# Optimization experiments

Measured on AMD Instinct MI355X. Metric: run time of the kernel, lower is better.

## Reference

```python
import jax, jax.numpy as jnp
import numpy as np

EPS = 1e-12

def _l2norm(x):
    # F.normalize(p=2, dim=-1) with torch's eps clamp
    n = jnp.sqrt(jnp.sum(x * x, axis=-1, keepdims=True))
    return x / jnp.maximum(n, EPS)

def setup_inputs() -> dict:
    key = jax.random.key(0)
    k1, k2, k3, k4 = jax.random.split(key, 4)
    B, Lq, Ld, H, D = 64, 32, 256, 768, 128
    Q_hidden = jax.random.normal(k1, (B, Lq, H), dtype=jnp.float32)
    D_hidden = jax.random.normal(k2, (B, Ld, H), dtype=jnp.float32)
    W = jax.random.normal(k3, (D, H), dtype=jnp.float32) * (1.0 / np.sqrt(H))
    d_mask = jax.random.randint(k4, (B, Ld), 0, 2).astype(bool)
    d_mask = d_mask.at[:, 0].set(True)  # every doc has >=1 valid token
    return {"Q_hidden": Q_hidden, "D_hidden": D_hidden, "W": W, "d_mask": d_mask}

def reference(Q_hidden, D_hidden, W, d_mask):
    # linear projection (no bias) + L2 normalize, as in query()/doc()
    Q = _l2norm(jnp.einsum('blh,dh->bld', Q_hidden, W))       # [B,Lq,D]
    Dv = _l2norm(jnp.einsum('blh,dh->bld', D_hidden, W))      # [B,Ld,D]
    Dv = Dv * d_mask[..., None].astype(Dv.dtype)              # zero padded/skiplist tokens
    # intra-batch cosine MaxSim: sim[b,c,q,n] = Q[b,q] . D[c,n]
    sim = jnp.einsum('bqd,cnd->bcqn', Q, Dv)                  # [B,B,Lq,Ld]
    sim = jnp.where(d_mask[None, :, None, :], sim, -jnp.inf)  # mask doc tokens
    return jnp.sum(jnp.max(sim, axis=-1), axis=-1)            # [B,B]
```

## Files before the change

### kernel.cpp

```cpp
#include <hip/hip_runtime.h>
#include <hip/hip_bf16.h>
#include <math.h>

typedef __attribute__((ext_vector_type(4))) float f32x4;
typedef __attribute__((ext_vector_type(8))) short bf16x8;

#define NB    64
#define LQ    32
#define LDOC  256
#define HDIM  768
#define DDIM  128
#define NTOK_Q (NB * LQ)
#define NTOK_D (NB * LDOC)
#define NTOK   (NTOK_Q + NTOK_D)

#define WS_OFF_W    0
#define WS_OFF_MASK 196608
#define WS_OFF_QN   212992
#define WS_OFF_DN   737280

__device__ inline short f2bf(float f) {
    unsigned u = __float_as_uint(f);
    u = (u + 0x7fffu + ((u >> 16) & 1u)) >> 16;
    return (short)u;
}

__global__ void prep(const float* __restrict__ W, short* __restrict__ Wbf,
                     const unsigned char* __restrict__ mraw,
                     unsigned short* __restrict__ maskT) {
    if (blockIdx.x < 96) {
        int i = blockIdx.x * 256 + threadIdx.x;
        float4 v = *(const float4*)(W + (size_t)i * 4);
        short4 o;
        o.x = f2bf(v.x); o.y = f2bf(v.y); o.z = f2bf(v.z); o.w = f2bf(v.w);
        *(short4*)(Wbf + (size_t)i * 4) = o;
        return;
    }
    __shared__ int dword_ok_s;
    if (threadIdx.x == 0) dword_ok_s = 1;
    __syncthreads();
    const unsigned* dw = (const unsigned*)mraw;
    int ok = 1;
    for (int i = threadIdx.x; i < 4096; i += 256) {
        unsigned v = dw[i];
        if (!(v == 0u || v == 1u || v == 0x3F800000u)) ok = 0;
    }
    if (!ok) atomicAnd(&dword_ok_s, 0);
    __syncthreads();
    const int isdw = dword_ok_s;
    for (int w = threadIdx.x; w < 1024; w += 256) {
        const int c = w >> 4, lcc = w & 15;
        unsigned bits = 0;
        if (isdw) {
            for (int nt = 0; nt < 16; ++nt)
                bits |= (dw[c * 256 + nt * 16 + lcc] ? 1u : 0u) << nt;
        } else {
            for (int nt = 0; nt < 16; ++nt)
                bits |= (mraw[c * 256 + nt * 16 + lcc] ? 1u : 0u) << nt;
        }
        maskT[w] = (unsigned short)bits;
    }
}

__global__ __launch_bounds__(256)
void proj_norm(const float* __restrict__ Qh, const float* __restrict__ Dh,
               const short* __restrict__ Wbf,
               short* __restrict__ Qn, short* __restrict__ Dn) {
    const int tid  = threadIdx.x;
    const int lane = tid & 63;
    const int wave = tid >> 6;
    const int g    = lane >> 4;
    const int lc   = lane & 15;
    const int wr   = wave >> 1;
    const int wc   = wave & 1;
    const int row0 = blockIdx.x * 64;

    const float* Asrc = (row0 < NTOK_Q) ? Qh + (size_t)row0 * HDIM
                                        : Dh + (size_t)(row0 - NTOK_Q) * HDIM;

    __shared__ alignas(16) float As[2][4096];
    __shared__ alignas(16) short Bs[2][8192];
    __shared__ float norms[2][2][32];

    auto STAGE = [&](int buf, int t) {
#pragma unroll
        for (int i = 0; i < 4; ++i) {
            const int sb = i * 256 + wave * 64;
            const int s  = sb + lane;
            const int row = s >> 4;
            const int cu  = (s & 15) ^ (row & 15);
            const float* ga = Asrc + (size_t)row * HDIM + t * 64 + cu * 4;
            __builtin_amdgcn_global_load_lds(
                (const __attribute__((address_space(1))) unsigned*)ga,
                (__attribute__((address_space(3))) unsigned*)((char*)&As[buf][0] + (size_t)sb * 16),
                16, 0, 0);
        }
#pragma unroll
        for (int i = 0; i < 4; ++i) {
            const int sb = i * 256 + wave * 64;
            const int s  = sb + lane;
            const int n  = s >> 3;
            const int c8 = (s & 7) ^ (n & 7);
            const short* gb = Wbf + (size_t)n * HDIM + t * 64 + c8 * 8;
            __builtin_amdgcn_global_load_lds(
                (const __attribute__((address_space(1))) unsigned*)gb,
                (__attribute__((address_space(3))) unsigned*)((char*)&Bs[buf][0] + (size_t)sb * 16),
                16, 0, 0);
        }
    };

    f32x4 acc[2][4];
#pragma unroll
    for (int m = 0; m < 2; ++m)
#pragma unroll
        for (int nt = 0; nt < 4; ++nt) acc[m][nt] = (f32x4){0.f, 0.f, 0.f, 0.f};

    STAGE(0, 0);
    __syncthreads();

    for (int t = 0; t < 12; ++t) {
        const int cur = t & 1;
        if (t < 11) STAGE(cur ^ 1, t + 1);

        const float* Ab = &As[cur][0];
        const short* Bb = &Bs[cur][0];
#pragma unroll
        for (int ks = 0; ks < 2; ++ks) {
            bf16x8 bfr[4];
#pragma unroll
            for (int nt = 0; nt < 4; ++nt) {
                const int nl = wc * 64 + nt * 16 + lc;
                const int c8 = (ks * 4 + g) ^ (nl & 7);
                bfr[nt] = *(const bf16x8*)(Bb + (size_t)nl * 64 + c8 * 8);
            }
#pragma unroll
            for (int m = 0; m < 2; ++m) {
                const int rl = wr * 32 + m * 16 + lc;
                const int u0 = (ks * 8 + g * 2) ^ lc;
                const int u1 = (ks * 8 + g * 2 + 1) ^ lc;
                const float4 a0 = *(const float4*)(Ab + (size_t)rl * 64 + u0 * 4);
                const float4 a1 = *(const float4*)(Ab + (size_t)rl * 64 + u1 * 4);
                bf16x8 af;
                af[0] = f2bf(a0.x); af[1] = f2bf(a0.y); af[2] = f2bf(a0.z); af[3] = f2bf(a0.w);
                af[4] = f2bf(a1.x); af[5] = f2bf(a1.y); af[6] = f2bf(a1.z); af[7] = f2bf(a1.w);
#pragma unroll
                for (int nt = 0; nt < 4; ++nt)
                    acc[m][nt] = __builtin_amdgcn_mfma_f32_16x16x32_bf16(af, bfr[nt], acc[m][nt], 0, 0, 0);
            }
        }
        __syncthreads();
    }

    float part[2][4];
#pragma unroll
    for (int m = 0; m < 2; ++m)
#pragma unroll
        for (int i = 0; i < 4; ++i) {
            float s = 0.f;
#pragma unroll
            for (int nt = 0; nt < 4; ++nt) s += acc[m][nt][i] * acc[m][nt][i];
            s += __shfl_xor(s, 1);
            s += __shfl_xor(s, 2);
            s += __shfl_xor(s, 4);
            s += __shfl_xor(s, 8);
            part[m][i] = s;
        }
    if (lc == 0) {
#pragma unroll
        for (int m = 0; m < 2; ++m)
#pragma unroll
            for (int i = 0; i < 4; ++i)
                norms[wr][wc][m * 16 + g * 4 + i] = part[m][i];
    }
    __syncthreads();

    short* Obase = (row0 < NTOK_Q) ? Qn + (size_t)row0 * DDIM
                                   : Dn + (size_t)(row0 - NTOK_Q) * DDIM;
#pragma unroll
    for (int m = 0; m < 2; ++m)
#pragma unroll
        for (int i = 0; i < 4; ++i) {
            const int rloc = m * 16 + g * 4 + i;
            const float tot = norms[wr][0][rloc] + norms[wr][1][rloc];
            const float inv = 1.f / fmaxf(sqrtf(tot), 1e-12f);
            short* dst = Obase + (size_t)(wr * 32 + rloc) * DDIM + wc * 64;
#pragma unroll
            for (int nt = 0; nt < 4; ++nt)
                dst[nt * 16 + lc] = f2bf(acc[m][nt][i] * inv);
        }
}

__global__ __launch_bounds__(256)
void maxsim(const short* __restrict__ Qn, const short* __restrict__ Dn,
            const unsigned short* __restrict__ maskT, float* __restrict__ out) {
    const int x  = blockIdx.x & 7;
    const int m8 = (blockIdx.x >> 3) & 7;
    const int bg = blockIdx.x >> 6;
    const int c  = x * 8 + m8;

    const int wave = threadIdx.x >> 6;
    const int lane = threadIdx.x & 63;
    const int g = lane >> 4, lc = lane & 15;

    __shared__ alignas(16) short Ds[LDOC * DDIM];

    const short* dsrc = Dn + (size_t)c * LDOC * DDIM;
#pragma unroll
    for (int i = 0; i < 16; ++i) {
        const int slot = wave * 1024 + i * 64 + lane;
        const int row = slot >> 4, c16 = slot & 15;
        const short* gaddr = dsrc + row * DDIM + ((c16 ^ (row & 15)) * 8);
        __builtin_amdgcn_global_load_lds(
            (const __attribute__((address_space(1))) unsigned int*)gaddr,
            (__attribute__((address_space(3))) unsigned int*)(Ds + (size_t)(wave * 1024 + i * 64) * 8),
            16, 0, 0);
    }

    bf16x8 qf[4][4];
    const int qrow0 = bg * 256 + wave * 64;
#pragma unroll
    for (int m = 0; m < 4; ++m) {
        const short* qb = Qn + (size_t)(qrow0 + m * 16 + lc) * DDIM;
#pragma unroll
        for (int ks = 0; ks < 4; ++ks)
            qf[m][ks] = *(const bf16x8*)(qb + ks * 32 + g * 8);
    }

    const unsigned mbits = maskT[c * 16 + lc];

    __syncthreads();

    float rmax[4][4];
#pragma unroll
    for (int m = 0; m < 4; ++m)
#pragma unroll
        for (int i = 0; i < 4; ++i) rmax[m][i] = -INFINITY;

    for (int nt = 0; nt < 16; ++nt) {
        bf16x8 bf[4];
        const int row = nt * 16 + lc;
#pragma unroll
        for (int ks = 0; ks < 4; ++ks) {
            const int c16 = (ks * 4 + g) ^ lc;
            bf[ks] = *(const bf16x8*)(Ds + row * DDIM + c16 * 8);
        }
        const bool on = (mbits >> nt) & 1;
#pragma unroll
        for (int m = 0; m < 4; ++m) {
            f32x4 acc = (f32x4){0.f, 0.f, 0.f, 0.f};
#pragma unroll
            for (int ks = 0; ks < 4; ++ks)
                acc = __builtin_amdgcn_mfma_f32_16x16x32_bf16(qf[m][ks], bf[ks], acc, 0, 0, 0);
#pragma unroll
            for (int i = 0; i < 4; ++i)
                rmax[m][i] = on ? fmaxf(rmax[m][i], acc[i]) : rmax[m][i];
        }
    }

    float s_lo = 0.f, s_hi = 0.f;
#pragma unroll
    for (int m = 0; m < 4; ++m) {
#pragma unroll
        for (int i = 0; i < 4; ++i) {
            float r = rmax[m][i];
            r = fmaxf(r, __shfl_xor(r, 1));
            r = fmaxf(r, __shfl_xor(r, 2));
            r = fmaxf(r, __shfl_xor(r, 4));
            r = fmaxf(r, __shfl_xor(r, 8));
            if (m < 2) s_lo += r; else s_hi += r;
        }
    }
    s_lo += __shfl_xor(s_lo, 16);
    s_lo += __shfl_xor(s_lo, 32);
    s_hi += __shfl_xor(s_hi, 16);
    s_hi += __shfl_xor(s_hi, 32);

    if (lane == 0) {
        const int b_lo = bg * 8 + wave * 2;
        out[(size_t)b_lo * NB + c]       = s_lo;
        out[(size_t)(b_lo + 1) * NB + c] = s_hi;
    }
}

extern "C" void kernel_launch(void* const* d_in, const int* in_sizes, int n_in,
                              void* d_out, int out_size, void* d_ws, size_t ws_size,
                              hipStream_t stream) {
    const float* Qh = (const float*)d_in[0];
    const float* Dh = (const float*)d_in[1];
    const float* W  = (const float*)d_in[2];
    const unsigned char* dm = (const unsigned char*)d_in[3];
    float* out = (float*)d_out;
    char* ws = (char*)d_ws;

    short*          Wbf   = (short*)(ws + WS_OFF_W);
    unsigned short* maskT = (unsigned short*)(ws + WS_OFF_MASK);
    short*          Qn    = (short*)(ws + WS_OFF_QN);
    short*          Dn    = (short*)(ws + WS_OFF_DN);

    prep<<<97, 256, 0, stream>>>(W, Wbf, dm, maskT);
    proj_norm<<<NTOK / 64, 256, 0, stream>>>(Qh, Dh, Wbf, Qn, Dn);
    maxsim<<<512, 256, 0, stream>>>(Qn, Dn, maskT, out);
}
```

Baseline: 50.36 us.

## Halve projection row tile and pipeline doc chunks in maxsim with 512 threads

proj_norm now processes 32 rows per block instead of 64, which doubles the grid (576 blocks) and roughly halves the A-tile LDS and accumulator registers. maxsim now uses 8 waves per block with 32 query rows each and streams the 256-token doc tile in four double-buffered 64-row chunks instead of loading the whole 64KB tile up front. The aim is more resident blocks and overlap of doc loads with MFMA work. In exchange, W-tile traffic per output row doubles in the projection, and maxsim adds per-chunk barriers.

Result: faster. 42.63 us (-15.4%).

```diff
diff --git a/kernel.cpp b/kernel.cpp
--- a/kernel.cpp
+++ b/kernel.cpp
@@ -73,18 +73,18 @@
     const int lc   = lane & 15;
     const int wr   = wave >> 1;
     const int wc   = wave & 1;
-    const int row0 = blockIdx.x * 64;
+    const int row0 = blockIdx.x * 32;
 
     const float* Asrc = (row0 < NTOK_Q) ? Qh + (size_t)row0 * HDIM
                                         : Dh + (size_t)(row0 - NTOK_Q) * HDIM;
 
-    __shared__ alignas(16) float As[2][4096];
+    __shared__ alignas(16) float As[2][2048];
     __shared__ alignas(16) short Bs[2][8192];
-    __shared__ float norms[2][2][32];
+    __shared__ float norms[2][2][16];
 
     auto STAGE = [&](int buf, int t) {
 #pragma unroll
-        for (int i = 0; i < 4; ++i) {
+        for (int i = 0; i < 2; ++i) {
             const int sb = i * 256 + wave * 64;
             const int s  = sb + lane;
             const int row = s >> 4;
@@ -109,11 +109,9 @@
         }
     };
 
-    f32x4 acc[2][4];
-#pragma unroll
-    for (int m = 0; m < 2; ++m)
-#pragma unroll
-        for (int nt = 0; nt < 4; ++nt) acc[m][nt] = (f32x4){0.f, 0.f, 0.f, 0.f};
+    f32x4 acc[4];
+#pragma unroll
+    for (int nt = 0; nt < 4; ++nt) acc[nt] = (f32x4){0.f, 0.f, 0.f, 0.f};
 
     STAGE(0, 0);
     __syncthreads();
@@ -133,64 +131,54 @@
                 const int c8 = (ks * 4 + g) ^ (nl & 7);
                 bfr[nt] = *(const bf16x8*)(Bb + (size_t)nl * 64 + c8 * 8);
             }
-#pragma unroll
-            for (int m = 0; m < 2; ++m) {
-                const int rl = wr * 32 + m * 16 + lc;
-                const int u0 = (ks * 8 + g * 2) ^ lc;
-                const int u1 = (ks * 8 + g * 2 + 1) ^ lc;
-                const float4 a0 = *(const float4*)(Ab + (size_t)rl * 64 + u0 * 4);
-                const float4 a1 = *(const float4*)(Ab + (size_t)rl * 64 + u1 * 4);
-                bf16x8 af;
-                af[0] = f2bf(a0.x); af[1] = f2bf(a0.y); af[2] = f2bf(a0.z); af[3] = f2bf(a0.w);
-                af[4] = f2bf(a1.x); af[5] = f2bf(a1.y); af[6] = f2bf(a1.z); af[7] = f2bf(a1.w);
-#pragma unroll
-                for (int nt = 0; nt < 4; ++nt)
-                    acc[m][nt] = __builtin_amdgcn_mfma_f32_16x16x32_bf16(af, bfr[nt], acc[m][nt], 0, 0, 0);
-            }
+            const int rl = wr * 16 + lc;
+            const int u0 = (ks * 8 + g * 2) ^ lc;
+            const int u1 = (ks * 8 + g * 2 + 1) ^ lc;
+            const float4 a0 = *(const float4*)(Ab + (size_t)rl * 64 + u0 * 4);
+            const float4 a1 = *(const float4*)(Ab + (size_t)rl * 64 + u1 * 4);
+            bf16x8 af;
+            af[0] = f2bf(a0.x); af[1] = f2bf(a0.y); af[2] = f2bf(a0.z); af[3] = f2bf(a0.w);
+            af[4] = f2bf(a1.x); af[5] = f2bf(a1.y); af[6] = f2bf(a1.z); af[7] = f2bf(a1.w);
+#pragma unroll
+            for (int nt = 0; nt < 4; ++nt)
+                acc[nt] = __builtin_amdgcn_mfma_f32_16x16x32_bf16(af, bfr[nt], acc[nt], 0, 0, 0);
         }
         __syncthreads();
     }
 
-    float part[2][4];
-#pragma unroll
-    for (int m = 0; m < 2; ++m)
-#pragma unroll
-        for (int i = 0; i < 4; ++i) {
-            float s = 0.f;
-#pragma unroll
-            for (int nt = 0; nt < 4; ++nt) s += acc[m][nt][i] * acc[m][nt][i];
-            s += __shfl_xor(s, 1);
-            s += __shfl_xor(s, 2);
-            s += __shfl_xor(s, 4);
-            s += __shfl_xor(s, 8);
-            part[m][i] = s;
-        }
+    float part[4];
+#pragma unroll
+    for (int i = 0; i < 4; ++i) {
+        float s = 0.f;
+#pragma unroll
+        for (int nt = 0; nt < 4; ++nt) s += acc[nt][i] * acc[nt][i];
+        s += __shfl_xor(s, 1);
+        s += __shfl_xor(s, 2);
+        s += __shfl_xor(s, 4);
+        s += __shfl_xor(s, 8);
+        part[i] = s;
+    }
     if (lc == 0) {
 #pragma unroll
-        for (int m = 0; m < 2; ++m)
-#pragma unroll
-            for (int i = 0; i < 4; ++i)
-                norms[wr][wc][m * 16 + g * 4 + i] = part[m][i];
+        for (int i = 0; i < 4; ++i) norms[wr][wc][g * 4 + i] = part[i];
     }
     __syncthreads();
 
     short* Obase = (row0 < NTOK_Q) ? Qn + (size_t)row0 * DDIM
                                    : Dn + (size_t)(row0 - NTOK_Q) * DDIM;
 #pragma unroll
-    for (int m = 0; m < 2; ++m)
-#pragma unroll
-        for (int i = 0; i < 4; ++i) {
-            const int rloc = m * 16 + g * 4 + i;
-            const float tot = norms[wr][0][rloc] + norms[wr][1][rloc];
-            const float inv = 1.f / fmaxf(sqrtf(tot), 1e-12f);
-            short* dst = Obase + (size_t)(wr * 32 + rloc) * DDIM + wc * 64;
-#pragma unroll
-            for (int nt = 0; nt < 4; ++nt)
-                dst[nt * 16 + lc] = f2bf(acc[m][nt][i] * inv);
-        }
-}
-
-__global__ __launch_bounds__(256)
+    for (int i = 0; i < 4; ++i) {
+        const int rloc = g * 4 + i;
+        const float tot = norms[wr][0][rloc] + norms[wr][1][rloc];
+        const float inv = 1.f / fmaxf(sqrtf(tot), 1e-12f);
+        short* dst = Obase + (size_t)(wr * 16 + rloc) * DDIM + wc * 64;
+#pragma unroll
+        for (int nt = 0; nt < 4; ++nt)
+            dst[nt * 16 + lc] = f2bf(acc[nt][i] * inv);
+    }
+}
+
+__global__ __launch_bounds__(512)
 void maxsim(const short* __restrict__ Qn, const short* __restrict__ Dn,
             const unsigned short* __restrict__ maskT, float* __restrict__ out) {
     const int x  = blockIdx.x & 7;
@@ -202,64 +190,77 @@
     const int lane = threadIdx.x & 63;
     const int g = lane >> 4, lc = lane & 15;
 
-    __shared__ alignas(16) short Ds[LDOC * DDIM];
+    __shared__ alignas(16) short Ds[2][4096 * 2];
 
     const short* dsrc = Dn + (size_t)c * LDOC * DDIM;
-#pragma unroll
-    for (int i = 0; i < 16; ++i) {
-        const int slot = wave * 1024 + i * 64 + lane;
-        const int row = slot >> 4, c16 = slot & 15;
-        const short* gaddr = dsrc + row * DDIM + ((c16 ^ (row & 15)) * 8);
-        __builtin_amdgcn_global_load_lds(
-            (const __attribute__((address_space(1))) unsigned int*)gaddr,
-            (__attribute__((address_space(3))) unsigned int*)(Ds + (size_t)(wave * 1024 + i * 64) * 8),
-            16, 0, 0);
-    }
-
-    bf16x8 qf[4][4];
-    const int qrow0 = bg * 256 + wave * 64;
-#pragma unroll
-    for (int m = 0; m < 4; ++m) {
+
+    auto STAGE = [&](int buf, int ch) {
+#pragma unroll
+        for (int i = 0; i < 2; ++i) {
+            const int sb = wave * 128 + i * 64;
+            const int s  = sb + lane;
+            const int rowl = s >> 4;
+            const int c16  = (s & 15) ^ (rowl & 15);
+            const short* ga = dsrc + (size_t)(ch * 64 + rowl) * DDIM + c16 * 8;
+            __builtin_amdgcn_global_load_lds(
+                (const __attribute__((address_space(1))) unsigned*)ga,
+                (__attribute__((address_space(3))) unsigned*)((char*)&Ds[buf][0] + (size_t)sb * 16),
+                16, 0, 0);
+        }
+    };
+
+    STAGE(0, 0);
+
+    bf16x8 qf[2][4];
+    const int qrow0 = bg * 256 + wave * 32;
+#pragma unroll
+    for (int m = 0; m < 2; ++m) {
         const short* qb = Qn + (size_t)(qrow0 + m * 16 + lc) * DDIM;
 #pragma unroll
         for (int ks = 0; ks < 4; ++ks)
             qf[m][ks] = *(const bf16x8*)(qb + ks * 32 + g * 8);
     }
-
     const unsigned mbits = maskT[c * 16 + lc];
 
     __syncthreads();
 
-    float rmax[4][4];
-#pragma unroll
-    for (int m = 0; m < 4; ++m)
+    float rmax[2][4];
+#pragma unroll
+    for (int m = 0; m < 2; ++m)
 #pragma unroll
         for (int i = 0; i < 4; ++i) rmax[m][i] = -INFINITY;
 
-    for (int nt = 0; nt < 16; ++nt) {
-        bf16x8 bf[4];
-        const int row = nt * 16 + lc;
-#pragma unroll
-        for (int ks = 0; ks < 4; ++ks) {
-            const int c16 = (ks * 4 + g) ^ lc;
-            bf[ks] = *(const bf16x8*)(Ds + row * DDIM + c16 * 8);
-        }
-        const bool on = (mbits >> nt) & 1;
-#pragma unroll
-        for (int m = 0; m < 4; ++m) {
-            f32x4 acc = (f32x4){0.f, 0.f, 0.f, 0.f};
-#pragma unroll
-            for (int ks = 0; ks < 4; ++ks)
-                acc = __builtin_amdgcn_mfma_f32_16x16x32_bf16(qf[m][ks], bf[ks], acc, 0, 0, 0);
-#pragma unroll
-            for (int i = 0; i < 4; ++i)
-                rmax[m][i] = on ? fmaxf(rmax[m][i], acc[i]) : rmax[m][i];
-        }
-    }
-
-    float s_lo = 0.f, s_hi = 0.f;
-#pragma unroll
-    for (int m = 0; m < 4; ++m) {
+    for (int ch = 0; ch < 4; ++ch) {
+        const int buf = ch & 1;
+        if (ch < 3) STAGE(buf ^ 1, ch + 1);
+        const short* Db = &Ds[buf][0];
+#pragma unroll
+        for (int j = 0; j < 4; ++j) {
+            const int rowl = j * 16 + lc;
+            bf16x8 bf[4];
+#pragma unroll
+            for (int ks = 0; ks < 4; ++ks) {
+                const int c16 = (ks * 4 + g) ^ lc;
+                bf[ks] = *(const bf16x8*)(Db + (size_t)rowl * DDIM + c16 * 8);
+            }
+            const bool on = (mbits >> (ch * 4 + j)) & 1;
+#pragma unroll
+            for (int m = 0; m < 2; ++m) {
+                f32x4 acc = (f32x4){0.f, 0.f, 0.f, 0.f};
+#pragma unroll
+                for (int ks = 0; ks < 4; ++ks)
+                    acc = __builtin_amdgcn_mfma_f32_16x16x32_bf16(qf[m][ks], bf[ks], acc, 0, 0, 0);
+#pragma unroll
+                for (int i = 0; i < 4; ++i)
+                    rmax[m][i] = on ? fmaxf(rmax[m][i], acc[i]) : rmax[m][i];
+            }
+        }
+        __syncthreads();
+    }
+
+    float s = 0.f;
+#pragma unroll
+    for (int m = 0; m < 2; ++m)
 #pragma unroll
         for (int i = 0; i < 4; ++i) {
             float r = rmax[m][i];
@@ -267,18 +268,14 @@
             r = fmaxf(r, __shfl_xor(r, 2));
             r = fmaxf(r, __shfl_xor(r, 4));
             r = fmaxf(r, __shfl_xor(r, 8));
-            if (m < 2) s_lo += r; else s_hi += r;
-        }
-    }
-    s_lo += __shfl_xor(s_lo, 16);
-    s_lo += __shfl_xor(s_lo, 32);
-    s_hi += __shfl_xor(s_hi, 16);
-    s_hi += __shfl_xor(s_hi, 32);
+            s += r;
+        }
+    s += __shfl_xor(s, 16);
+    s += __shfl_xor(s, 32);
 
     if (lane == 0) {
-        const int b_lo = bg * 8 + wave * 2;
-        out[(size_t)b_lo * NB + c]       = s_lo;
-        out[(size_t)(b_lo + 1) * NB + c] = s_hi;
+        const int b = bg * 8 + wave;
+        out[(size_t)b * NB + c] = s;
     }
 }
 
@@ -298,6 +295,6 @@
     short*          Dn    = (short*)(ws + WS_OFF_DN);
 
     prep<<<97, 256, 0, stream>>>(W, Wbf, dm, maskT);
-    proj_norm<<<NTOK / 64, 256, 0, stream>>>(Qh, Dh, Wbf, Qn, Dn);
-    maxsim<<<512, 256, 0, stream>>>(Qn, Dn, maskT, out);
-}
+    proj_norm<<<NTOK / 32, 256, 0, stream>>>(Qh, Dh, Wbf, Qn, Dn);
+    maxsim<<<512, 512, 0, stream>>>(Qn, Dn, maskT, out);
+}
```
